# Kernel tuning notes

Hardware: AMD Instinct MI355X
Metric: run time of the kernel (lower is better)

Reference implementation:

```python
import jax, jax.numpy as jnp
import numpy as np

NUM_HEADS = 16
D_MODEL = 1024


def setup_inputs() -> dict:
    key = jax.random.key(0)
    k1, k2, k3 = jax.random.split(key, 3)
    x = jax.random.normal(k1, (4, 2048, D_MODEL), dtype=jnp.float32)
    # torch.nn.Linear weights are [out_features, in_features]
    w_qkv = jax.random.normal(k2, (3 * D_MODEL, D_MODEL), dtype=jnp.float32) * (1.0 / np.sqrt(D_MODEL))
    w_o = jax.random.normal(k3, (D_MODEL, D_MODEL), dtype=jnp.float32) * (1.0 / np.sqrt(D_MODEL))
    return {"x": x, "w_qkv": w_qkv, "w_o": w_o}


def reference(x, w_qkv, w_o):
    b, n, _ = x.shape
    h = NUM_HEADS
    dh = D_MODEL // h  # head dim
    qkv = jnp.einsum('bnd,ed->bne', x, w_qkv)            # (b, n, 3*d_model)
    # Faithful to: rearrange(qkv, 'b n (h d) -> b h n d', h=h) then chunk(3, dim=-1)
    qkv = qkv.reshape(b, n, h, 3 * dh).transpose(0, 2, 1, 3)  # (b, h, n, 3*dh)
    q, k, v = jnp.split(qkv, 3, axis=-1)                 # each (b, h, n, dh)
    scale = 1.0 / jnp.sqrt(jnp.asarray(dh, dtype=x.dtype))
    scores = jnp.einsum('bhqd,bhkd->bhqk', q, k) * scale  # (b, h, n, n)
    attn = jax.nn.softmax(scores, axis=-1)
    out = jnp.einsum('bhqk,bhkd->bhqd', attn, v)          # (b, h, n, dh)
    out = out.transpose(0, 2, 1, 3).reshape(b, n, h * dh)  # 'b h n d -> b n (h d)'
    return jnp.einsum('bnd,ed->bne', out, w_o)
```

## Files before the change

kernel.cpp:

```cpp
#include <hip/hip_runtime.h>

#define BATCH 4
#define SEQ 2048
#define DM 1024
#define NH 16
#define DH 64
#define M_TOT (BATCH * SEQ)
#define EQKV (3 * DM)
#define QSCALE 0.18033688011112042f

typedef __bf16 bf16x8 __attribute__((ext_vector_type(8)));
typedef unsigned short u16x8 __attribute__((ext_vector_type(8)));
typedef float f32x4 __attribute__((ext_vector_type(4)));
typedef float f32x16 __attribute__((ext_vector_type(16)));

static __device__ __forceinline__ unsigned short f2bf(float f) {
    unsigned int u = __builtin_bit_cast(unsigned int, f);
    u += 0x7fffu + ((u >> 16) & 1u);
    return (unsigned short)(u >> 16);
}

static __device__ __forceinline__ unsigned int pkbf(float a, float b) {
#if __has_builtin(__builtin_amdgcn_cvt_pk_bf16_f32)
    typedef __bf16 bf16x2 __attribute__((ext_vector_type(2)));
    bf16x2 r = __builtin_amdgcn_cvt_pk_bf16_f32(a, b);
    return __builtin_bit_cast(unsigned int, r);
#else
    return (unsigned int)f2bf(a) | ((unsigned int)f2bf(b) << 16);
#endif
}

static __device__ __forceinline__ float fast_exp2(float x) {
#if __has_builtin(__builtin_amdgcn_exp2f)
    return __builtin_amdgcn_exp2f(x);
#else
    return exp2f(x);
#endif
}

static __device__ __forceinline__ bf16x8 ld_frag(const ushort* p) {
    return *(const bf16x8*)p;
}

static __device__ __forceinline__ bf16x8 mk_frag(unsigned int a, unsigned int b,
                                                 unsigned int c, unsigned int d) {
    union { unsigned int u[4]; bf16x8 v; } t;
    t.u[0] = a; t.u[1] = b; t.u[2] = c; t.u[3] = d;
    return t.v;
}

__global__ __launch_bounds__(256) void detect_kernel(const ushort* __restrict__ x,
                                                     int* __restrict__ flag) {
    __shared__ int cnt[256];
    const int tid = threadIdx.x;
    int c = 0;
    for (int j = 0; j < 16; ++j) {
        unsigned short w = x[tid * 16 + j];
        int e = (w >> 7) & 0xFF;
        bool sane = (e == 0) || (e >= 0x60 && e <= 0x8F);
        c += sane ? 0 : 1;
    }
    cnt[tid] = c;
    __syncthreads();
    for (int s = 128; s > 0; s >>= 1) {
        if (tid < s) cnt[tid] += cnt[tid + s];
        __syncthreads();
    }
    if (tid == 0) flag[0] = (cnt[0] > 256) ? 1 : 0;
}

__global__ __launch_bounds__(256) void convert_frag_kernel(
    const void* __restrict__ src, ushort* __restrict__ dst, int R,
    const int* __restrict__ flag)
{
    const int t = blockIdx.x * 256 + threadIdx.x;
    if (t >= R * 128) return;
    const int m = t >> 7, kc = t & 127;

    u16x8 v;
    if (flag[0]) {
        const float* s = (const float*)src + (size_t)t * 8;
        #pragma unroll
        for (int j = 0; j < 8; ++j) v[j] = f2bf(s[j]);
    } else {
        v = *((const u16x8*)src + t);
    }
    const size_t o = (((size_t)(m >> 4) * 32 + (kc >> 2)) * 64 + (kc & 3) * 16 + (m & 15)) * 8;
    *(u16x8*)(dst + o) = v;
}

__global__ __launch_bounds__(256) void qkv_gemm_kernel(
    const ushort* __restrict__ XF, const ushort* __restrict__ WF,
    ushort* __restrict__ QF, ushort* __restrict__ KF, ushort* __restrict__ VF)
{
    const int lane = threadIdx.x & 63;
    const int wave = threadIdx.x >> 6;
    const int col  = lane & 15;
    const int quad = lane >> 4;
    const int m0 = blockIdx.y * 128 + (wave >> 1) * 64;
    const int e0 = blockIdx.x * 128 + (wave & 1) * 64;
    const int mt0 = m0 >> 4, et0 = e0 >> 4;

    f32x4 acc[4][4];
    #pragma unroll
    for (int i = 0; i < 4; ++i)
        #pragma unroll
        for (int j = 0; j < 4; ++j) acc[i][j] = f32x4{0.f, 0.f, 0.f, 0.f};

    for (int kt = 0; kt < 32; ++kt) {
        bf16x8 a[4], b[4];
        #pragma unroll
        for (int i = 0; i < 4; ++i) {
            a[i] = ld_frag(XF + ((size_t)((mt0 + i) * 32 + kt) * 64 + lane) * 8);
            b[i] = ld_frag(WF + ((size_t)((et0 + i) * 32 + kt) * 64 + lane) * 8);
        }
        #pragma unroll
        for (int i = 0; i < 4; ++i)
            #pragma unroll
            for (int j = 0; j < 4; ++j)
                acc[i][j] = __builtin_amdgcn_mfma_f32_16x16x32_bf16(a[i], b[j], acc[i][j], 0, 0, 0);
    }

    #pragma unroll
    for (int ej = 0; ej < 4; ++ej) {
        const int e = e0 + ej * 16 + col;
        const int h = e / 192;
        const int c = e - h * 192;
        #pragma unroll
        for (int mi = 0; mi < 4; ++mi) {
            #pragma unroll
            for (int r = 0; r < 4; ++r) {
                const int m = m0 + mi * 16 + quad * 4 + r;
                const int bh = (m >> 11) * NH + h;
                const int n = m & (SEQ - 1);
                const float val = acc[mi][ej][r];
                if (c < 64) {
                    const int d = c;
                    QF[(((size_t)(bh * 64 + (n >> 5)) * 4 + (d >> 4)) * 64
                        + ((d >> 3) & 1) * 32 + (n & 31)) * 8 + (d & 7)] = f2bf(val * QSCALE);
                } else if (c < 128) {
                    const int d = c - 64;
                    KF[(((size_t)(bh * 64 + (n >> 5)) * 4 + (d >> 4)) * 64
                        + ((d >> 3) & 1) * 32 + (n & 31)) * 8 + (d & 7)] = f2bf(val);
                } else {
                    const int d = c - 128;
                    VF[((((size_t)(bh * 32 + (n >> 6)) * 2 + (d >> 5)) * 4 + ((n >> 4) & 3)) * 64
                        + ((n >> 3) & 1) * 32 + (d & 31)) * 8 + (n & 7)] = f2bf(val);
                }
            }
        }
    }
}

__global__ __launch_bounds__(256) void attn_kernel(
    const ushort* __restrict__ QF, const ushort* __restrict__ KF,
    const ushort* __restrict__ VF, ushort* __restrict__ AOF)
{
    const int lane = threadIdx.x & 63;
    const int wave = threadIdx.x >> 6;
    const int half = lane >> 5;
    const int l31  = lane & 31;

    const int i = blockIdx.x;
    const int xcd = i & 7;
    const int s = i >> 3;
    const int qt4 = s & 15;
    const int bh = ((s >> 4) << 3) | xcd;
    const int q0 = qt4 * 128 + wave * 32;

    const ushort* qfb = QF + ((size_t)(bh * 64 + (q0 >> 5)) * 4) * 512;
    bf16x8 bq[4];
    #pragma unroll
    for (int d4 = 0; d4 < 4; ++d4) bq[d4] = ld_frag(qfb + d4 * 512 + lane * 8);

    const ushort* kfb = KF + (size_t)bh * 64 * 4 * 512;
    const ushort* vfb = VF + (size_t)bh * 32 * 8 * 512;

    float l_i = 0.f;
    f32x16 acc0 = {}, acc1 = {};

    for (int kv0 = 0; kv0 < SEQ; kv0 += 64) {
        const ushort* vp = vfb + (size_t)(kv0 >> 6) * 8 * 512;
        bf16x8 va0[4], va1[4];
        #pragma unroll
        for (int f4 = 0; f4 < 4; ++f4) {
            va0[f4] = ld_frag(vp + f4 * 512 + lane * 8);
            va1[f4] = ld_frag(vp + (4 + f4) * 512 + lane * 8);
        }

        f32x16 st0 = {}, st1 = {};
        const ushort* kp = kfb + (size_t)(kv0 >> 5) * 4 * 512;
        #pragma unroll
        for (int d4 = 0; d4 < 4; ++d4) {
            bf16x8 ka0 = ld_frag(kp + d4 * 512 + lane * 8);
            bf16x8 ka1 = ld_frag(kp + (4 + d4) * 512 + lane * 8);
            st0 = __builtin_amdgcn_mfma_f32_32x32x16_bf16(ka0, bq[d4], st0, 0, 0, 0);
            st1 = __builtin_amdgcn_mfma_f32_32x32x16_bf16(ka1, bq[d4], st1, 0, 0, 0);
        }

        float rs = 0.f;
        #pragma unroll
        for (int t = 0; t < 16; ++t) { st0[t] = fast_exp2(st0[t]); rs += st0[t]; }
        #pragma unroll
        for (int t = 0; t < 16; ++t) { st1[t] = fast_exp2(st1[t]); rs += st1[t]; }
        l_i += rs;

        unsigned int u[16], ex[16];
        #pragma unroll
        for (int t = 0; t < 8; ++t) u[t]     = pkbf(st0[2 * t], st0[2 * t + 1]);
        #pragma unroll
        for (int t = 0; t < 8; ++t) u[8 + t] = pkbf(st1[2 * t], st1[2 * t + 1]);
        #pragma unroll
        for (int t = 0; t < 16; ++t) ex[t] = __shfl_xor(u[t], 32, 64);

        bf16x8 pf[4];
        pf[0] = half == 0 ? mk_frag(u[0], u[1], ex[0], ex[1])     : mk_frag(ex[2], ex[3], u[2], u[3]);
        pf[1] = half == 0 ? mk_frag(u[4], u[5], ex[4], ex[5])     : mk_frag(ex[6], ex[7], u[6], u[7]);
        pf[2] = half == 0 ? mk_frag(u[8], u[9], ex[8], ex[9])     : mk_frag(ex[10], ex[11], u[10], u[11]);
        pf[3] = half == 0 ? mk_frag(u[12], u[13], ex[12], ex[13]) : mk_frag(ex[14], ex[15], u[14], u[15]);

        #pragma unroll
        for (int f4 = 0; f4 < 4; ++f4) {
            acc0 = __builtin_amdgcn_mfma_f32_32x32x16_bf16(va0[f4], pf[f4], acc0, 0, 0, 0);
            acc1 = __builtin_amdgcn_mfma_f32_32x32x16_bf16(va1[f4], pf[f4], acc1, 0, 0, 0);
        }
    }

    l_i += __shfl_xor(l_i, 32, 64);

    const int b = bh >> 4, h = bh & (NH - 1);
    const float inv = 1.f / l_i;
    const int n_g = b * SEQ + q0 + l31;
    #pragma unroll
    for (int r = 0; r < 16; ++r) {
        const int d = (r & 3) + 8 * (r >> 2) + 4 * half;
        #pragma unroll
        for (int p = 0; p < 2; ++p) {
            const int e = h * 64 + p * 32 + d;
            const float val = (p == 0 ? acc0[r] : acc1[r]) * inv;
            AOF[(((size_t)(n_g >> 4) * 32 + (e >> 5)) * 64
                 + ((e >> 3) & 3) * 16 + (n_g & 15)) * 8 + (e & 7)] = f2bf(val);
        }
    }
}

__global__ __launch_bounds__(256) void out_gemm_kernel(
    const ushort* __restrict__ AOF, const ushort* __restrict__ WOF,
    void* __restrict__ out, const int* __restrict__ flag)
{
    const int lane = threadIdx.x & 63;
    const int wave = threadIdx.x >> 6;
    const int col  = lane & 15;
    const int quad = lane >> 4;
    const int m0 = blockIdx.y * 128 + (wave >> 1) * 64;
    const int e0 = blockIdx.x * 128 + (wave & 1) * 64;
    const int mt0 = m0 >> 4, et0 = e0 >> 4;
    const int f = flag[0];

    f32x4 acc[4][4];
    #pragma unroll
    for (int i = 0; i < 4; ++i)
        #pragma unroll
        for (int j = 0; j < 4; ++j) acc[i][j] = f32x4{0.f, 0.f, 0.f, 0.f};

    for (int kt = 0; kt < 32; ++kt) {
        bf16x8 a[4], b[4];
        #pragma unroll
        for (int i = 0; i < 4; ++i) {
            a[i] = ld_frag(AOF + ((size_t)((mt0 + i) * 32 + kt) * 64 + lane) * 8);
            b[i] = ld_frag(WOF + ((size_t)((et0 + i) * 32 + kt) * 64 + lane) * 8);
        }
        #pragma unroll
        for (int i = 0; i < 4; ++i)
            #pragma unroll
            for (int j = 0; j < 4; ++j)
                acc[i][j] = __builtin_amdgcn_mfma_f32_16x16x32_bf16(a[i], b[j], acc[i][j], 0, 0, 0);
    }

    if (f == 0) {
        ushort* o = (ushort*)out;
        #pragma unroll
        for (int mi = 0; mi < 4; ++mi)
            #pragma unroll
            for (int ej = 0; ej < 4; ++ej)
                #pragma unroll
                for (int r = 0; r < 4; ++r)
                    o[(size_t)(m0 + mi * 16 + quad * 4 + r) * DM + e0 + ej * 16 + col] = f2bf(acc[mi][ej][r]);
    } else {
        float* o = (float*)out;
        #pragma unroll
        for (int mi = 0; mi < 4; ++mi)
            #pragma unroll
            for (int ej = 0; ej < 4; ++ej)
                #pragma unroll
                for (int r = 0; r < 4; ++r)
                    o[(size_t)(m0 + mi * 16 + quad * 4 + r) * DM + e0 + ej * 16 + col] = acc[mi][ej][r];
    }
}

extern "C" void kernel_launch(void* const* d_in, const int* in_sizes, int n_in,
                              void* d_out, int out_size, void* d_ws, size_t ws_size,
                              hipStream_t stream) {
    const void* x_raw     = d_in[0];
    const void* w_qkv_raw = d_in[1];
    const void* w_o_raw   = d_in[2];

    char* ws = (char*)d_ws;
    int*    flag  = (int*)ws;
    ushort* XF    = (ushort*)(ws + 256);
    ushort* WQKVF = (ushort*)(ws + 256 + (16u << 20));
    ushort* WOF   = (ushort*)(ws + 256 + (22u << 20));
    ushort* QF    = (ushort*)(ws + 256 + (24u << 20));
    ushort* KF    = (ushort*)(ws + 256 + (40u << 20));
    ushort* VF    = (ushort*)(ws + 256 + (56u << 20));
    ushort* AOF   = XF;

    detect_kernel<<<1, 256, 0, stream>>>((const ushort*)x_raw, flag);
    convert_frag_kernel<<<M_TOT / 2, 256, 0, stream>>>(x_raw, XF, M_TOT, flag);
    convert_frag_kernel<<<EQKV / 2, 256, 0, stream>>>(w_qkv_raw, WQKVF, EQKV, flag);
    convert_frag_kernel<<<DM / 2, 256, 0, stream>>>(w_o_raw, WOF, DM, flag);

    qkv_gemm_kernel<<<dim3(EQKV / 128, M_TOT / 128), 256, 0, stream>>>(XF, WQKVF, QF, KF, VF);
    attn_kernel<<<dim3(BATCH * NH * (SEQ / 128)), 256, 0, stream>>>(QF, KF, VF, AOF);
    out_gemm_kernel<<<dim3(DM / 128, M_TOT / 128), 256, 0, stream>>>(AOF, WOF, d_out, flag);
}
```

Baseline: 334.8 us.

## Split attention KV range across wave pairs and reduce partials in LDS

Each block now handles 64 queries instead of 128, and the four waves split into two query tiles times two halves of the KV sequence. Each wave loops over 1024 keys instead of 2048, and partial accumulators and row sums are combined through shared memory before normalising and writing. This doubles the grid size and halves the per-wave serial loop, to shorten the critical path and improve occupancy. In exchange it adds an LDS reduction and a barrier, and each K/V block is loaded by twice as many blocks overall. Skipping the running max stays valid because the base code uses no max subtraction either.

```diff
diff --git a/kernel.cpp b/kernel.cpp
--- a/kernel.cpp
+++ b/kernel.cpp
@@ -156,6 +156,8 @@
     const ushort* __restrict__ QF, const ushort* __restrict__ KF,
     const ushort* __restrict__ VF, ushort* __restrict__ AOF)
 {
+    __shared__ float lred[2][33][64];
+
     const int lane = threadIdx.x & 63;
     const int wave = threadIdx.x >> 6;
     const int half = lane >> 5;
@@ -164,23 +166,25 @@
     const int i = blockIdx.x;
     const int xcd = i & 7;
     const int s = i >> 3;
-    const int qt4 = s & 15;
-    const int bh = ((s >> 4) << 3) | xcd;
-    const int q0 = qt4 * 128 + wave * 32;
+    const int qc = s & 31;
+    const int bh = ((s >> 5) << 3) | xcd;
+    const int qt  = wave & 1;
+    const int kvh = wave >> 1;
+    const int q0 = qc * 64 + qt * 32;
 
     const ushort* qfb = QF + ((size_t)(bh * 64 + (q0 >> 5)) * 4) * 512;
     bf16x8 bq[4];
     #pragma unroll
     for (int d4 = 0; d4 < 4; ++d4) bq[d4] = ld_frag(qfb + d4 * 512 + lane * 8);
 
-    const ushort* kfb = KF + (size_t)bh * 64 * 4 * 512;
-    const ushort* vfb = VF + (size_t)bh * 32 * 8 * 512;
+    const ushort* kfb = KF + (size_t)bh * 131072 + (size_t)kvh * 65536;
+    const ushort* vfb = VF + (size_t)bh * 131072 + (size_t)kvh * 65536;
 
     float l_i = 0.f;
     f32x16 acc0 = {}, acc1 = {};
 
-    for (int kv0 = 0; kv0 < SEQ; kv0 += 64) {
-        const ushort* vp = vfb + (size_t)(kv0 >> 6) * 8 * 512;
+    for (int it = 0; it < 16; ++it) {
+        const ushort* vp = vfb + (size_t)it * 4096;
         bf16x8 va0[4], va1[4];
         #pragma unroll
         for (int f4 = 0; f4 < 4; ++f4) {
@@ -189,7 +193,7 @@
         }
 
         f32x16 st0 = {}, st1 = {};
-        const ushort* kp = kfb + (size_t)(kv0 >> 5) * 4 * 512;
+        const ushort* kp = kfb + (size_t)it * 4096;
         #pragma unroll
         for (int d4 = 0; d4 < 4; ++d4) {
             bf16x8 ka0 = ld_frag(kp + d4 * 512 + lane * 8);
@@ -228,18 +232,36 @@
 
     l_i += __shfl_xor(l_i, 32, 64);
 
-    const int b = bh >> 4, h = bh & (NH - 1);
-    const float inv = 1.f / l_i;
-    const int n_g = b * SEQ + q0 + l31;
-    #pragma unroll
-    for (int r = 0; r < 16; ++r) {
-        const int d = (r & 3) + 8 * (r >> 2) + 4 * half;
-        #pragma unroll
-        for (int p = 0; p < 2; ++p) {
-            const int e = h * 64 + p * 32 + d;
-            const float val = (p == 0 ? acc0[r] : acc1[r]) * inv;
-            AOF[(((size_t)(n_g >> 4) * 32 + (e >> 5)) * 64
-                 + ((e >> 3) & 3) * 16 + (n_g & 15)) * 8 + (e & 7)] = f2bf(val);
+    if (kvh == 1) {
+        #pragma unroll
+        for (int r = 0; r < 16; ++r) {
+            lred[qt][r][lane]      = acc0[r];
+            lred[qt][16 + r][lane] = acc1[r];
+        }
+        lred[qt][32][lane] = l_i;
+    }
+    __syncthreads();
+    if (kvh == 0) {
+        #pragma unroll
+        for (int r = 0; r < 16; ++r) {
+            acc0[r] += lred[qt][r][lane];
+            acc1[r] += lred[qt][16 + r][lane];
+        }
+        l_i += lred[qt][32][lane];
+
+        const int b = bh >> 4, h = bh & (NH - 1);
+        const float inv = 1.f / l_i;
+        const int n_g = b * SEQ + q0 + l31;
+        #pragma unroll
+        for (int r = 0; r < 16; ++r) {
+            const int d = (r & 3) + 8 * (r >> 2) + 4 * half;
+            #pragma unroll
+            for (int p = 0; p < 2; ++p) {
+                const int e = h * 64 + p * 32 + d;
+                const float val = (p == 0 ? acc0[r] : acc1[r]) * inv;
+                AOF[(((size_t)(n_g >> 4) * 32 + (e >> 5)) * 64
+                     + ((e >> 3) & 3) * 16 + (n_g & 15)) * 8 + (e & 7)] = f2bf(val);
+            }
         }
     }
 }
@@ -321,6 +343,6 @@
     convert_frag_kernel<<<DM / 2, 256, 0, stream>>>(w_o_raw, WOF, DM, flag);
 
     qkv_gemm_kernel<<<dim3(EQKV / 128, M_TOT / 128), 256, 0, stream>>>(XF, WQKVF, QF, KF, VF);
-    attn_kernel<<<dim3(BATCH * NH * (SEQ / 128)), 256, 0, stream>>>(QF, KF, VF, AOF);
+    attn_kernel<<<dim3(BATCH * NH * (SEQ / 64)), 256, 0, stream>>>(QF, KF, VF, AOF);
     out_gemm_kernel<<<dim3(DM / 128, M_TOT / 128), 256, 0, stream>>>(AOF, WOF, d_out, flag);
 }
```

After: 320.9 us. 1.04x faster.
